# Performance work log

Measured on AMD Instinct MI355X. Metric: run time of the kernel, lower is better.

Reference implementation:

```python
import jax, jax.numpy as jnp
import numpy as np

HEADS = 16
DIM_HEAD = 64

def setup_inputs() -> dict:
    key = jax.random.key(0)
    ks = jax.random.split(key, 5)
    B, S, D = 2, 2048, 1024
    return {
        "hidden_states": jax.random.normal(ks[0], (B, S, D), dtype=jnp.float32),
        "Wq": jax.random.normal(ks[1], (D, D), dtype=jnp.float32) * (D ** -0.5),
        "Wkv": jax.random.normal(ks[2], (D, D), dtype=jnp.float32) * (D ** -0.5),
        "Wout": jax.random.normal(ks[3], (D, D), dtype=jnp.float32) * (D ** -0.5),
        "bout": jnp.zeros((D,), dtype=jnp.float32),
    }

def reference(hidden_states, Wq, Wkv, Wout, bout):
    B, S, D = hidden_states.shape
    H, Dh = HEADS, DIM_HEAD
    # projections (torch Linear: x @ W.T; here weights are stored as [in, out])
    q = hidden_states @ Wq            # [B, S, D]
    kv = hidden_states @ Wkv          # key == value share the to_kv projection
    q = q.reshape(B, S, H, Dh).transpose(0, 2, 1, 3)   # [B, H, S, Dh]
    k = kv.reshape(B, S, H, Dh).transpose(0, 2, 1, 3)
    v = k
    scale = 1.0 / np.sqrt(Dh).astype(np.float32)
    # ReLU attention: no softmax
    attn = jax.nn.relu(jnp.einsum("bhsd,bhtd->bhst", q, k) * scale)  # [B,H,S,S]
    out = jnp.einsum("bhst,bhtd->bhsd", attn, v)                     # [B,H,S,Dh]
    out = out.transpose(0, 2, 1, 3).reshape(B, S, H * Dh)
    return out @ Wout + bout
```

## Files before the change

### kernel.cpp

```cpp
#include <hip/hip_runtime.h>
#include <hip/hip_bf16.h>

#define HEADS  16
#define DIMH   64
#define NBATCH 2
#define SEQ    2048
#define DMODEL 1024
#define MROWS  (NBATCH * SEQ)

typedef __attribute__((ext_vector_type(8)))  short bf16x8;
typedef __attribute__((ext_vector_type(4)))  float f32x4;
typedef __attribute__((ext_vector_type(16))) float f32x16;
typedef __attribute__((ext_vector_type(4)))  float float4v;
typedef __attribute__((ext_vector_type(4)))  short short4v;

__device__ inline void glds16(const void* g, void* l) {
    __builtin_amdgcn_global_load_lds(
        (const __attribute__((address_space(1))) unsigned int*)g,
        (__attribute__((address_space(3))) unsigned int*)l, 16, 0, 0);
}

#define WAIT_VMCNT(N) asm volatile("s_waitcnt vmcnt(" #N ")" ::: "memory")
#define BARRIER() do { __builtin_amdgcn_s_barrier(); asm volatile("" ::: "memory"); } while (0)

__global__ void cvt_kernel(const float* __restrict__ in,
                           __hip_bfloat16* __restrict__ out, int n4) {
    int i = blockIdx.x * blockDim.x + threadIdx.x;
    if (i >= n4) return;
    float4v v = reinterpret_cast<const float4v*>(in)[i];
    union { short4v s; __hip_bfloat16 h[4]; } u;
#pragma unroll
    for (int j = 0; j < 4; ++j) u.h[j] = __float2bfloat16(v[j]);
    reinterpret_cast<short4v*>(out)[i] = u.s;
}

__global__ void tr_kernel(const float* __restrict__ W,
                          __hip_bfloat16* __restrict__ WT) {
    __shared__ float tile[32][33];
    int i = blockIdx.y * 32 + threadIdx.y;
    int o = blockIdx.x * 32 + threadIdx.x;
    tile[threadIdx.y][threadIdx.x] = W[i * DMODEL + o];
    __syncthreads();
    int oo = blockIdx.x * 32 + threadIdx.y;
    int ii = blockIdx.y * 32 + threadIdx.x;
    WT[oo * DMODEL + ii] = __float2bfloat16(tile[threadIdx.x][threadIdx.y]);
}


__launch_bounds__(512, 2)
__global__ void proj_kernel(const __hip_bfloat16* __restrict__ hsb,
                            const __hip_bfloat16* __restrict__ WqT,
                            const __hip_bfloat16* __restrict__ WkvT,
                            __hip_bfloat16* __restrict__ qb,
                            __hip_bfloat16* __restrict__ kb,
                            __hip_bfloat16* __restrict__ vtb) {
    __shared__ __align__(16) char SLDS[73728];
    char (*Alds)[8192]  = (char (*)[8192])SLDS;
    char (*Blds)[16384] = (char (*)[16384])(SLDS + 24576);
    char* CT = SLDS;

    const int tid  = threadIdx.x;
    const int wave = tid >> 6;
    const int lane = tid & 63;
    const int lr = lane & 15;
    const int lk = lane >> 4;
    const int wm = wave >> 2, wn = wave & 3;

    int bid = blockIdx.x;
    bid = (bid & 7) * 32 + (bid >> 3);
    const int xt = bid & 7;
    const int mt = bid >> 3;
    const bool is_q = xt < 4;
    const int mbase = mt * 128;
    const int nbase = (xt & 3) * 256;
    const __hip_bfloat16* __restrict__ WT = is_q ? WqT : WkvT;

    const char* __restrict__ Ab = (const char*)(hsb + (size_t)mbase * DMODEL);
    const char* __restrict__ Bb = (const char*)(WT + (size_t)nbase * DMODEL);

    auto stage = [&](int buf, int k0) {
        const size_t colb = (size_t)k0 * 2 + lk * 16;
        glds16(Ab + (size_t)(wave * 16 + lr) * (DMODEL * 2) + colb,
               &Alds[buf][wave * 1024]);
#pragma unroll
        for (int r = 0; r < 2; ++r)
            glds16(Bb + (size_t)((r * 8 + wave) * 16 + lr) * (DMODEL * 2) + colb,
                   &Blds[buf][r * 8192 + wave * 1024]);
    };

    stage(0, 0);
    stage(1, 32);

    f32x4 acc[4][4] = {};
    int c0 = 0;
    for (int t = 0; t < DMODEL / 32; ++t) {
        if (t < DMODEL / 32 - 1) WAIT_VMCNT(3); else WAIT_VMCNT(0);
        BARRIER();
        if (t + 2 < DMODEL / 32) {
            int sb = c0 + 2; if (sb >= 3) sb -= 3;
            stage(sb, (t + 2) * 32);
        }
        bf16x8 af[4], bfr[4];
#pragma unroll
        for (int i = 0; i < 4; ++i) {
            af[i]  = *reinterpret_cast<const bf16x8*>(&Alds[c0][(wm * 4 + i) * 1024 + lane * 16]);
            bfr[i] = *reinterpret_cast<const bf16x8*>(&Blds[c0][(wn * 4 + i) * 1024 + lane * 16]);
        }
#pragma unroll
        for (int i = 0; i < 4; ++i)
#pragma unroll
            for (int j = 0; j < 4; ++j)
                acc[i][j] = __builtin_amdgcn_mfma_f32_16x16x32_bf16(af[i], bfr[j], acc[i][j], 0, 0, 0);
        c0 = (c0 + 1 == 3) ? 0 : c0 + 1;
    }

    const float qscale = is_q ? 0.125f : 1.0f;
    const int b_ = mbase >> 11;
    const int s0 = mbase & (SEQ - 1);
    BARRIER();

#pragma unroll
    for (int i = 0; i < 4; ++i)
#pragma unroll
        for (int j = 0; j < 4; ++j)
#pragma unroll
            for (int r = 0; r < 4; ++r) {
                int m = wm * 64 + i * 16 + lk * 4 + r;
                int n = wn * 64 + j * 16 + lr;
                *reinterpret_cast<__hip_bfloat16*>(
                    &CT[m * 512 + ((n * 2) ^ (((m >> 2) & 7) << 4))]) =
                    __float2bfloat16(acc[i][j][r] * qscale);
            }
    BARRIER();

    __hip_bfloat16* __restrict__ dst0 = is_q ? qb : kb;
#pragma unroll
    for (int p = 0; p < 8; ++p) {
        int g = p * 64 + (tid >> 3);
        int m = g >> 2, seg = g & 3, o = tid & 7;
        int key = ((m >> 2) & 7) << 4;
        bf16x8 val = *reinterpret_cast<const bf16x8*>(
            &CT[m * 512 + ((seg * 128 + o * 16) ^ key)]);
        int h = (nbase >> 6) + seg;
        *reinterpret_cast<bf16x8*>(
            &dst0[(((size_t)b_ * HEADS + h) * SEQ + s0 + m) * DIMH + o * 8]) = val;
    }

    if (!is_q) {
        BARRIER();
#pragma unroll
        for (int i = 0; i < 4; ++i)
#pragma unroll
            for (int j = 0; j < 4; ++j)
#pragma unroll
                for (int r = 0; r < 4; ++r) {
                    int m = wm * 64 + i * 16 + lk * 4 + r;
                    int n = wn * 64 + j * 16 + lr;
                    *reinterpret_cast<__hip_bfloat16*>(
                        &CT[n * 256 + ((m * 2) ^ ((n & 7) << 4))]) =
                        __float2bfloat16(acc[i][j][r]);
                }
        BARRIER();
#pragma unroll
        for (int p = 0; p < 8; ++p) {
            int g = p * 64 + (tid >> 3);
            int n = g >> 1, half = g & 1, o = tid & 7;
            int key2 = (n & 7) << 4;
            bf16x8 val = *reinterpret_cast<const bf16x8*>(
                &CT[n * 256 + ((half * 128 + o * 16) ^ key2)]);
            int h = (nbase >> 6) + (n >> 6);
            int dh = n & 63;
            *reinterpret_cast<bf16x8*>(
                &vtb[(((size_t)b_ * HEADS + h) * DIMH + dh) * SEQ + s0 + half * 64 + o * 8]) = val;
        }
    }
}

__launch_bounds__(512, 2)
__global__ void outproj_kernel(const __hip_bfloat16* __restrict__ ao,
                               const __hip_bfloat16* __restrict__ WoT,
                               const float* __restrict__ bout,
                               float* __restrict__ out) {
    __shared__ __align__(16) char Alds[3][8192];
    __shared__ __align__(16) char Blds[3][8192];
    const int tid  = threadIdx.x;
    const int wave = tid >> 6;
    const int lane = tid & 63;
    const int lr = lane & 15;
    const int lk = lane >> 4;
    const int wm = wave >> 1, wn = wave & 1;

    int bid = blockIdx.x;
    bid = (bid & 7) * 32 + (bid >> 3);
    const int xt = bid & 7;
    const int mt = bid >> 3;
    const int mbase = mt * 128;
    const int nbase = xt * 128;

    const char* __restrict__ Ab = (const char*)(ao + (size_t)mbase * DMODEL);
    const char* __restrict__ Bb = (const char*)(WoT + (size_t)nbase * DMODEL);

    auto stage = [&](int buf, int k0) {
        const size_t colb = (size_t)k0 * 2 + lk * 16;
        glds16(Ab + (size_t)(wave * 16 + lr) * (DMODEL * 2) + colb,
               &Alds[buf][wave * 1024]);
        glds16(Bb + (size_t)(wave * 16 + lr) * (DMODEL * 2) + colb,
               &Blds[buf][wave * 1024]);
    };

    stage(0, 0);
    stage(1, 32);

    f32x4 acc[2][4] = {};
    int c0 = 0;
    for (int t = 0; t < DMODEL / 32; ++t) {
        if (t < DMODEL / 32 - 1) WAIT_VMCNT(2); else WAIT_VMCNT(0);
        BARRIER();
        if (t + 2 < DMODEL / 32) {
            int sb = c0 + 2; if (sb >= 3) sb -= 3;
            stage(sb, (t + 2) * 32);
        }
        bf16x8 af[2], bfr[4];
#pragma unroll
        for (int i = 0; i < 2; ++i)
            af[i] = *reinterpret_cast<const bf16x8*>(&Alds[c0][(wm * 2 + i) * 1024 + lane * 16]);
#pragma unroll
        for (int j = 0; j < 4; ++j)
            bfr[j] = *reinterpret_cast<const bf16x8*>(&Blds[c0][(wn * 4 + j) * 1024 + lane * 16]);
#pragma unroll
        for (int i = 0; i < 2; ++i)
#pragma unroll
            for (int j = 0; j < 4; ++j)
                acc[i][j] = __builtin_amdgcn_mfma_f32_16x16x32_bf16(af[i], bfr[j], acc[i][j], 0, 0, 0);
        c0 = (c0 + 1 == 3) ? 0 : c0 + 1;
    }

#pragma unroll
    for (int j = 0; j < 4; ++j) {
        const int n = nbase + wn * 64 + j * 16 + lr;
        const float bias = bout[n];
#pragma unroll
        for (int i = 0; i < 2; ++i) {
#pragma unroll
            for (int r = 0; r < 4; ++r) {
                int m = mbase + wm * 32 + i * 16 + lk * 4 + r;
                out[(size_t)m * DMODEL + n] = acc[i][j][r] + bias;
            }
        }
    }
}

__launch_bounds__(256, 2)
__global__ void attn_kernel(const __hip_bfloat16* __restrict__ qb,
                            const __hip_bfloat16* __restrict__ kb,
                            const __hip_bfloat16* __restrict__ vtb,
                            __hip_bfloat16* __restrict__ ao) {
    __shared__ __align__(16) char Klds[3][8192];
    __shared__ __align__(16) char Vlds[3][8192];
    const int lane = threadIdx.x & 63;
    const int wave = threadIdx.x >> 6;
    const int l32  = lane & 31;
    const int hi   = lane >> 5;

    int bid = blockIdx.x;
    bid = (bid & 7) * 64 + (bid >> 3);
    const int bh   = bid >> 4;
    const int qblk = bid & 15;
    const int b_ = bh >> 4, h = bh & 15;
    const int qbase = qblk * 128 + wave * 32;

    const __hip_bfloat16* __restrict__ Q = qb + (size_t)bh * SEQ * DIMH;
    const char* __restrict__ Kg = (const char*)(kb  + (size_t)bh * SEQ * DIMH);
    const char* __restrict__ Vg = (const char*)(vtb + (size_t)bh * DIMH * SEQ);

    bf16x8 qf[4];
#pragma unroll
    for (int ks = 0; ks < 4; ++ks)
        qf[ks] = *reinterpret_cast<const bf16x8*>(
            &Q[(size_t)(qbase + l32) * DIMH + ks * 16 + hi * 8]);

    f32x16 acco[2] = {};

    auto stage = [&](int buf, int t0) {
#pragma unroll
        for (int pass = 0; pass < 2; ++pass) {
            const int b   = wave * 2048 + pass * 1024 + lane * 16;
            const int row = b >> 7;
            const int cb  = (b & 127) ^ ((row & 7) << 4);
            glds16(Kg + (size_t)(t0 + row) * 128 + cb,
                   &Klds[buf][wave * 2048 + pass * 1024]);
            glds16(Vg + (size_t)row * (SEQ * 2) + t0 * 2 + cb,
                   &Vlds[buf][wave * 2048 + pass * 1024]);
        }
    };

    stage(0, 0);
    stage(1, 64);

    const int swz = (l32 & 7) << 4;
    int c0 = 0;
    for (int t0 = 0; t0 < SEQ; t0 += 64) {
        if (t0 + 64 < SEQ) WAIT_VMCNT(4); else WAIT_VMCNT(0);
        BARRIER();
        if (t0 + 128 < SEQ) {
            int sb = c0 + 2; if (sb >= 3) sb -= 3;
            stage(sb, t0 + 128);
        }
        const char* Kc = Klds[c0];
        const char* Vc = Vlds[c0];

        f32x16 s0 = {}, s1 = {};
#pragma unroll
        for (int ks = 0; ks < 4; ++ks) {
            bf16x8 k0f = *reinterpret_cast<const bf16x8*>(
                Kc + l32 * 128        + ((ks * 32 + 16 * hi) ^ swz));
            bf16x8 k1f = *reinterpret_cast<const bf16x8*>(
                Kc + (32 + l32) * 128 + ((ks * 32 + 16 * hi) ^ swz));
            s0 = __builtin_amdgcn_mfma_f32_32x32x16_bf16(k0f, qf[ks], s0, 0, 0, 0);
            s1 = __builtin_amdgcn_mfma_f32_32x32x16_bf16(k1f, qf[ks], s1, 0, 0, 0);
        }
#pragma unroll
        for (int r = 0; r < 16; ++r) {
            s0[r] = fmaxf(s0[r], 0.f);
            s1[r] = fmaxf(s1[r], 0.f);
        }
#pragma unroll
        for (int kt = 0; kt < 4; ++kt) {
            union { __hip_bfloat16 hh[8]; bf16x8 v; } pa;
            const int rb = (kt & 1) * 8;
#pragma unroll
            for (int j = 0; j < 8; ++j)
                pa.hh[j] = __float2bfloat16(kt < 2 ? s0[rb + j] : s1[rb + j]);
#pragma unroll
            for (int nt = 0; nt < 2; ++nt) {
                const int row = nt * 32 + l32;
                union { unsigned long long d[2]; bf16x8 v; } vb;
                vb.d[0] = *reinterpret_cast<const unsigned long long*>(
                    Vc + row * 128 + ((kt * 32 + 8 * hi) ^ swz));
                vb.d[1] = *reinterpret_cast<const unsigned long long*>(
                    Vc + row * 128 + ((kt * 32 + 16 + 8 * hi) ^ swz));
                acco[nt] = __builtin_amdgcn_mfma_f32_32x32x16_bf16(pa.v, vb.v, acco[nt], 0, 0, 0);
            }
        }
        c0 = (c0 + 1 == 3) ? 0 : c0 + 1;
    }

#pragma unroll
    for (int nt = 0; nt < 2; ++nt) {
#pragma unroll
        for (int r = 0; r < 16; ++r) {
            int q = qbase + (r & 3) + 8 * (r >> 2) + 4 * hi;
            ao[(size_t)(b_ * SEQ + q) * DMODEL + h * 64 + nt * 32 + l32] =
                __float2bfloat16(acco[nt][r]);
        }
    }
}

extern "C" void kernel_launch(void* const* d_in, const int* in_sizes, int n_in,
                              void* d_out, int out_size, void* d_ws, size_t ws_size,
                              hipStream_t stream) {
    const float* hs   = (const float*)d_in[0];
    const float* Wq   = (const float*)d_in[1];
    const float* Wkv  = (const float*)d_in[2];
    const float* Wout = (const float*)d_in[3];
    const float* bout = (const float*)d_in[4];
    float* out = (float*)d_out;

    char* ws = (char*)d_ws;
    size_t off = 0;
    auto alloc = [&](size_t bytes) { char* p = ws + off; off += bytes; return p; };
    __hip_bfloat16* hsb  = (__hip_bfloat16*)alloc((size_t)MROWS * DMODEL * 2);
    __hip_bfloat16* WqT  = (__hip_bfloat16*)alloc((size_t)DMODEL * DMODEL * 2);
    __hip_bfloat16* WkvT = (__hip_bfloat16*)alloc((size_t)DMODEL * DMODEL * 2);
    __hip_bfloat16* WoT  = (__hip_bfloat16*)alloc((size_t)DMODEL * DMODEL * 2);
    __hip_bfloat16* qb   = (__hip_bfloat16*)alloc((size_t)MROWS * DMODEL * 2);
    __hip_bfloat16* kb   = (__hip_bfloat16*)alloc((size_t)MROWS * DMODEL * 2);
    __hip_bfloat16* vtb  = (__hip_bfloat16*)alloc((size_t)MROWS * DMODEL * 2);
    __hip_bfloat16* ao   = hsb;

    cvt_kernel<<<(MROWS * DMODEL / 4 + 255) / 256, 256, 0, stream>>>(hs, hsb, MROWS * DMODEL / 4);
    dim3 trg(32, 32), trb(32, 32);
    tr_kernel<<<trg, trb, 0, stream>>>(Wq, WqT);
    tr_kernel<<<trg, trb, 0, stream>>>(Wkv, WkvT);
    tr_kernel<<<trg, trb, 0, stream>>>(Wout, WoT);

    proj_kernel<<<256, 512, 0, stream>>>(hsb, WqT, WkvT, qb, kb, vtb);

    attn_kernel<<<NBATCH * HEADS * (SEQ / 128), 256, 0, stream>>>(qb, kb, vtb, ao);

    outproj_kernel<<<256, 512, 0, stream>>>(ao, WoT, bout, out);
}
```

Before: 120.6 us.

## Software-pipeline attention loop: overlap QK of next tile with PV of previous

Restructures the attention inner loop so the QK^T MFMAs for tile t are issued after the PV MFMAs for tile t-1, giving the scheduler independent MFMA chains to interleave. LDS buffering grows from three to four stages so a V tile stays resident one iteration longer, and ReLU is folded into the bf16 pack. s_setprio is raised around the MFMA sections to favour compute waves. The extra LDS (64KB per block) may limit occupancy alongside the two-blocks launch bound.

```diff
diff --git a/kernel.cpp b/kernel.cpp
--- a/kernel.cpp
+++ b/kernel.cpp
@@ -255,8 +255,8 @@
                             const __hip_bfloat16* __restrict__ kb,
                             const __hip_bfloat16* __restrict__ vtb,
                             __hip_bfloat16* __restrict__ ao) {
-    __shared__ __align__(16) char Klds[3][8192];
-    __shared__ __align__(16) char Vlds[3][8192];
+    __shared__ __align__(16) char Klds[4][8192];
+    __shared__ __align__(16) char Vlds[4][8192];
     const int lane = threadIdx.x & 63;
     const int wave = threadIdx.x >> 6;
     const int l32  = lane & 31;
@@ -278,8 +278,6 @@
     for (int ks = 0; ks < 4; ++ks)
         qf[ks] = *reinterpret_cast<const bf16x8*>(
             &Q[(size_t)(qbase + l32) * DIMH + ks * 16 + hi * 8]);
-
-    f32x16 acco[2] = {};
 
     auto stage = [&](int buf, int t0) {
 #pragma unroll
@@ -294,43 +292,36 @@
         }
     };
 
-    stage(0, 0);
-    stage(1, 64);
-
     const int swz = (l32 & 7) << 4;
-    int c0 = 0;
-    for (int t0 = 0; t0 < SEQ; t0 += 64) {
-        if (t0 + 64 < SEQ) WAIT_VMCNT(4); else WAIT_VMCNT(0);
-        BARRIER();
-        if (t0 + 128 < SEQ) {
-            int sb = c0 + 2; if (sb >= 3) sb -= 3;
-            stage(sb, t0 + 128);
-        }
-        const char* Kc = Klds[c0];
-        const char* Vc = Vlds[c0];
-
-        f32x16 s0 = {}, s1 = {};
+    f32x16 acco[2] = {};
+    f32x16 sp0, sp1;
+
+    auto do_qk = [&](const char* Kc) {
+        sp0 = f32x16{}; sp1 = f32x16{};
+        __builtin_amdgcn_s_setprio(1);
 #pragma unroll
         for (int ks = 0; ks < 4; ++ks) {
             bf16x8 k0f = *reinterpret_cast<const bf16x8*>(
                 Kc + l32 * 128        + ((ks * 32 + 16 * hi) ^ swz));
             bf16x8 k1f = *reinterpret_cast<const bf16x8*>(
                 Kc + (32 + l32) * 128 + ((ks * 32 + 16 * hi) ^ swz));
-            s0 = __builtin_amdgcn_mfma_f32_32x32x16_bf16(k0f, qf[ks], s0, 0, 0, 0);
-            s1 = __builtin_amdgcn_mfma_f32_32x32x16_bf16(k1f, qf[ks], s1, 0, 0, 0);
-        }
-#pragma unroll
-        for (int r = 0; r < 16; ++r) {
-            s0[r] = fmaxf(s0[r], 0.f);
-            s1[r] = fmaxf(s1[r], 0.f);
-        }
+            sp0 = __builtin_amdgcn_mfma_f32_32x32x16_bf16(k0f, qf[ks], sp0, 0, 0, 0);
+            sp1 = __builtin_amdgcn_mfma_f32_32x32x16_bf16(k1f, qf[ks], sp1, 0, 0, 0);
+        }
+        __builtin_amdgcn_s_setprio(0);
+    };
+
+    auto do_packpv = [&](const char* Vc) {
+        __builtin_amdgcn_s_setprio(1);
 #pragma unroll
         for (int kt = 0; kt < 4; ++kt) {
             union { __hip_bfloat16 hh[8]; bf16x8 v; } pa;
             const int rb = (kt & 1) * 8;
 #pragma unroll
-            for (int j = 0; j < 8; ++j)
-                pa.hh[j] = __float2bfloat16(kt < 2 ? s0[rb + j] : s1[rb + j]);
+            for (int j = 0; j < 8; ++j) {
+                float x = (kt < 2) ? sp0[rb + j] : sp1[rb + j];
+                pa.hh[j] = __float2bfloat16(fmaxf(x, 0.f));
+            }
 #pragma unroll
             for (int nt = 0; nt < 2; ++nt) {
                 const int row = nt * 32 + l32;
@@ -342,8 +333,25 @@
                 acco[nt] = __builtin_amdgcn_mfma_f32_32x32x16_bf16(pa.v, vb.v, acco[nt], 0, 0, 0);
             }
         }
-        c0 = (c0 + 1 == 3) ? 0 : c0 + 1;
-    }
+        __builtin_amdgcn_s_setprio(0);
+    };
+
+    stage(0, 0);
+    stage(1, 64);
+
+    WAIT_VMCNT(4);
+    BARRIER();
+    stage(2, 128);
+    do_qk(Klds[0]);
+
+    for (int t = 1; t < SEQ / 64; ++t) {
+        if (t < SEQ / 64 - 1) WAIT_VMCNT(4); else WAIT_VMCNT(0);
+        BARRIER();
+        if (t + 2 < SEQ / 64) stage((t + 2) & 3, (t + 2) * 64);
+        do_packpv(Vlds[(t - 1) & 3]);
+        do_qk(Klds[t & 3]);
+    }
+    do_packpv(Vlds[(SEQ / 64 - 1) & 3]);
 
 #pragma unroll
     for (int nt = 0; nt < 2; ++nt) {
```

Result: faster. 118.1 us (-2.1%).
